# Performance work log

Hardware: AMD Instinct MI355X
Metric: run time of the kernel (lower is better)

## Reference

```python
import jax, jax.numpy as jnp
import numpy as np

DOF = 7
HID = 30
L_DIM = DOF * (DOF + 1) // 2  # 28
BATCH = 262144


def _linear_params(key, d_in, d_out, scale=0.3):
    k1, k2 = jax.random.split(key)
    W = jax.random.normal(k1, (d_out, d_in), dtype=jnp.float32) * scale / np.sqrt(d_in)
    b = jax.random.normal(k2, (d_out,), dtype=jnp.float32) * 0.01
    return W, b


def setup_inputs() -> dict:
    key = jax.random.key(0)
    ks = jax.random.split(key, 11)
    x = jax.random.normal(ks[0], (BATCH, 3 * DOF), dtype=jnp.float32)
    ld_w1, ld_b1 = _linear_params(ks[1], DOF, HID)
    ld_w2, ld_b2 = _linear_params(ks[2], HID, DOF)
    lo_w1, lo_b1 = _linear_params(ks[3], DOF, HID)
    lo_w2, lo_b2 = _linear_params(ks[4], HID, L_DIM - DOF)
    g_w1, g_b1 = _linear_params(ks[5], DOF, HID)
    g_w2, g_b2 = _linear_params(ks[6], HID, DOF)
    m_w1, m_b1 = _linear_params(ks[7], L_DIM + DOF, HID)
    m_w2, m_b2 = _linear_params(ks[8], HID, DOF)
    c_w1, c_b1 = _linear_params(ks[9], L_DIM * DOF + DOF, HID)
    c_w2, c_b2 = _linear_params(ks[10], HID, DOF)
    return dict(x=x,
                ld_w1=ld_w1, ld_b1=ld_b1, ld_w2=ld_w2, ld_b2=ld_b2,
                lo_w1=lo_w1, lo_b1=lo_b1, lo_w2=lo_w2, lo_b2=lo_b2,
                g_w1=g_w1, g_b1=g_b1, g_w2=g_w2, g_b2=g_b2,
                m_w1=m_w1, m_b1=m_b1, m_w2=m_w2, m_b2=m_b2,
                c_w1=c_w1, c_b1=c_b1, c_w2=c_w2, c_b2=c_b2)


def _sin_net_with_jac(q, W1, b1, W2, b2):
    # 2-layer SinNet: out = W2 @ sin(W1 q + b1) + b2, plus analytic batched Jacobian.
    pre = q @ W1.T + b1                 # [B, H]
    out = jnp.sin(pre) @ W2.T + b2      # [B, O]
    # d out_o / d q_d = sum_h W2[o,h] * cos(pre)[b,h] * W1[h,d]
    jac = jnp.einsum('oh,bh,hd->bod', W2, jnp.cos(pre), W1)  # [B, O, DOF]
    return out, jac


def _sigmoid_net(z, W1, b1, W2, b2):
    return jax.nn.sigmoid(z @ W1.T + b1) @ W2.T + b2


def reference(x,
              ld_w1, ld_b1, ld_w2, ld_b2,
              lo_w1, lo_b1, lo_w2, lo_b2,
              g_w1, g_b1, g_w2, g_b2,
              m_w1, m_b1, m_w2, m_b2,
              c_w1, c_b1, c_w2, c_b2):
    q = x[:, :DOF]
    qDot = x[:, DOF:2 * DOF]
    qDDot = x[:, 2 * DOF:3 * DOF]

    h_ld, jac_ld = _sin_net_with_jac(q, ld_w1, ld_b1, ld_w2, ld_b2)  # [B,DOF], [B,DOF,DOF]
    h_lo, jac_lo = _sin_net_with_jac(q, lo_w1, lo_b1, lo_w2, lo_b2)  # [B,L-D], [B,L-D,DOF]

    h_l = jnp.concatenate([h_ld, h_lo], axis=1)          # [B, L_DIM]
    m = _sigmoid_net(jnp.concatenate([h_l, qDDot], axis=1), m_w1, m_b1, m_w2, m_b2)

    # dl[:, i*DOF:(i+1)*DOF] = d h_l[:, i] / d q  -> flatten [B, L_DIM, DOF]
    dl = jnp.concatenate([jac_ld, jac_lo], axis=1).reshape(x.shape[0], L_DIM * DOF)
    c = _sigmoid_net(jnp.concatenate([dl, qDot], axis=1), c_w1, c_b1, c_w2, c_b2)

    g = jnp.sin(q @ g_w1.T + g_b1) @ g_w2.T + g_b2
    return m + c + g
```

## Files before the change

kernel.cpp:

```cpp
#include <hip/hip_runtime.h>


#define NT 256

typedef short bf16x8 __attribute__((ext_vector_type(8)));
typedef float f32x4  __attribute__((ext_vector_type(4)));

__device__ inline unsigned short f2b(float f) {
    union { float f; unsigned u; } v; v.f = f;
    return (unsigned short)((v.u + 0x7FFF + ((v.u >> 16) & 1)) >> 16);
}
__device__ inline unsigned pk2(float lo, float hi) {
    return (unsigned)f2b(lo) | ((unsigned)f2b(hi) << 16);
}

#define INV2PI 0.15915494309189535f

constexpr int PW_LD = 0;
constexpr int PW_LO = 1024;
constexpr int PW_G  = 2048;
constexpr int PB_MZ = 3072;
constexpr int PB_CZ = 6144;
constexpr int PB_O  = 9216;
constexpr int NPACK = 10752;

__global__ void precompute_kernel(
    const float* __restrict__ ld_w1, const float* __restrict__ ld_b1,
    const float* __restrict__ ld_w2, const float* __restrict__ ld_b2,
    const float* __restrict__ lo_w1, const float* __restrict__ lo_b1,
    const float* __restrict__ lo_w2, const float* __restrict__ lo_b2,
    const float* __restrict__ g_w1,  const float* __restrict__ g_b1,
    const float* __restrict__ g_w2,  const float* __restrict__ g_b2,
    const float* __restrict__ m_w1,  const float* __restrict__ m_b1,
    const float* __restrict__ m_w2,  const float* __restrict__ m_b2,
    const float* __restrict__ c_w1,  const float* __restrict__ c_b1,
    const float* __restrict__ c_w2,  const float* __restrict__ c_b2,
    float* __restrict__ ws)
{
    int i = blockIdx.x * blockDim.x + threadIdx.x;
    if (i < 16) { ws[i] = (i < 7) ? (m_b2[i] + c_b2[i] + g_b2[i]) : 0.f; return; }
    int r = i - 16;
    if (r >= NPACK) return;
    unsigned short* wp = (unsigned short*)ws + 32;
    float val = 0.f;
    if (r < 3072) {
        int tb = r / 1024, rr = r % 1024;
        int nc = rr >> 9, n = (rr >> 5) & 15, k = rr & 31, h = nc * 16 + n;
        const float* W1 = (tb == 0) ? ld_w1 : (tb == 1) ? lo_w1 : g_w1;
        const float* B1 = (tb == 0) ? ld_b1 : (tb == 1) ? lo_b1 : g_b1;
        if (h < 30) { if (k < 7) val = W1[h*7 + k]; else if (k == 7) val = B1[h]; }
    } else if (r < 6144) {
        int rr = r - 3072; int kc = rr >> 10; rr &= 1023;
        int nc = rr >> 9, n = (rr >> 5) & 15, k = rr & 31, j = nc * 16 + n;
        if (j < 30) {
            if (kc == 0) {
                if (k < 30) { float a = 0.f;
                    for (int o = 0; o < 7; ++o) a += m_w1[j*35 + o] * ld_w2[o*30 + k];
                    val = a; }
            } else if (kc == 1) {
                if (k < 30) { float a = 0.f;
                    for (int o = 0; o < 21; ++o) a += m_w1[j*35 + 7 + o] * lo_w2[o*30 + k];
                    val = a; }
            } else {
                if (k < 7) val = m_w1[j*35 + 28 + k];
                else if (k == 7) { float a = m_b1[j];
                    for (int o = 0; o < 7;  ++o) a += m_w1[j*35 + o]     * ld_b2[o];
                    for (int o = 0; o < 21; ++o) a += m_w1[j*35 + 7 + o] * lo_b2[o];
                    val = a; }
            }
        }
    } else if (r < 9216) {
        int rr = r - 6144; int kc = rr >> 10; rr &= 1023;
        int nc = rr >> 9, n = (rr >> 5) & 15, k = rr & 31, j = nc * 16 + n;
        if (j < 30) {
            if (kc == 0) {
                if (k < 30) { float a = 0.f;
                    for (int o = 0; o < 7; ++o) { float t = 0.f;
                        for (int d = 0; d < 7; ++d) t += c_w1[j*203 + o*7 + d] * ld_w1[k*7 + d];
                        a += ld_w2[o*30 + k] * t; }
                    val = a; }
            } else if (kc == 1) {
                if (k < 30) { float a = 0.f;
                    for (int o = 0; o < 21; ++o) { float t = 0.f;
                        for (int d = 0; d < 7; ++d) t += c_w1[j*203 + (7+o)*7 + d] * lo_w1[k*7 + d];
                        a += lo_w2[o*30 + k] * t; }
                    val = a; }
            } else {
                if (k < 7) val = c_w1[j*203 + 196 + k];
                else if (k == 7) val = c_b1[j];
            }
        }
    } else {
        int rr = r - 9216; int kc = rr >> 9, n = (rr >> 5) & 15, k = rr & 31;
        if (n < 7 && k < 30)
            val = ((kc == 0) ? m_w2 : (kc == 1) ? c_w2 : g_w2)[n*30 + k];
    }
    wp[r] = f2b(val);
}

#define MFMA(a, b, c) __builtin_amdgcn_mfma_f32_16x16x32_bf16((a), (b), (c), 0, 0, 0)

__global__ __launch_bounds__(NT, 3) void delan_main(
    const float* __restrict__ x, const float* __restrict__ ws, float* __restrict__ out)
{
    __shared__ __align__(16) unsigned short xs2[NT * 24 + 32];
    __shared__ __align__(16) unsigned short Lbuf[4 * 3968];

    const int tid = threadIdx.x;
    const int lane = tid & 63, wid = tid >> 6;
    const int n15 = lane & 15, quad = lane >> 4;

    {
        const float* xp = x + (size_t)(blockIdx.x * NT + tid) * 21;
        float v[21];
#pragma unroll
        for (int d = 0; d < 21; ++d) v[d] = xp[d];
        int4* dst = (int4*)(xs2 + tid * 24);
#pragma unroll
        for (int g = 0; g < 3; ++g) {
            int4 u;
            u.x = (int)pk2(v[g*7 + 0], v[g*7 + 1]);
            u.y = (int)pk2(v[g*7 + 2], v[g*7 + 3]);
            u.z = (int)pk2(v[g*7 + 4], v[g*7 + 5]);
            u.w = (int)pk2(v[g*7 + 6], 1.0f);
            dst[g] = u;
        }
    }
    if (tid < 16) ((unsigned*)(xs2 + NT * 24))[tid] = 0;
    __syncthreads();

    unsigned short* Ls = Lbuf + wid * 3968;
    unsigned short* Lc = Ls + 1152;
    unsigned short* Lg = Ls + 2304;

    const unsigned short* wp = (const unsigned short*)ws + 32;
    const int fo = n15 * 32 + quad * 8;

    bf16x8 bw_ld[2], bw_lo[2], bw_g[2], bm[3][2], bc[3][2], bo[3];
#pragma unroll
    for (int c = 0; c < 2; ++c) {
        bw_ld[c] = *(const bf16x8*)(wp + PW_LD + c*512 + fo);
        bw_lo[c] = *(const bf16x8*)(wp + PW_LO + c*512 + fo);
        bw_g[c]  = *(const bf16x8*)(wp + PW_G  + c*512 + fo);
#pragma unroll
        for (int kc = 0; kc < 3; ++kc) {
            bm[kc][c] = *(const bf16x8*)(wp + PB_MZ + kc*1024 + c*512 + fo);
            bc[kc][c] = *(const bf16x8*)(wp + PB_CZ + kc*1024 + c*512 + fo);
        }
    }
#pragma unroll
    for (int kc = 0; kc < 3; ++kc)
        bo[kc] = *(const bf16x8*)(wp + PB_O + kc*512 + fo);
    const float bout = ws[n15];

    const f32x4 zero4 = {0.f, 0.f, 0.f, 0.f};

    f32x4 pld[2], plo[2], pg[2];

    {
        const unsigned short* ep0 = xs2 + (wid * 64 + n15) * 24;
        bf16x8 a0 = *(const bf16x8*)(ep0 + quad * 8);
#pragma unroll
        for (int c = 0; c < 2; ++c) {
            pld[c] = MFMA(a0, bw_ld[c], zero4);
            plo[c] = MFMA(a0, bw_lo[c], zero4);
            pg[c]  = MFMA(a0, bw_g[c],  zero4);
        }
    }

#pragma unroll
    for (int t = 0; t < 4; ++t) {
        const int elb = wid * 64 + t * 16;
        const unsigned short* ep = xs2 + (elb + n15) * 24;

#pragma unroll
        for (int c = 0; c < 2; ++c) {
            const int h = c * 16 + n15;
#pragma unroll
            for (int rg = 0; rg < 4; ++rg) {
                const int m = quad * 4 + rg;
                float r1 = pld[c][rg] * INV2PI;
                Ls[m*72 + h]       = f2b(__builtin_amdgcn_sinf(r1));
                Lc[m*72 + h]       = f2b(__builtin_amdgcn_cosf(r1));
                float r2 = plo[c][rg] * INV2PI;
                Ls[m*72 + 32 + h]  = f2b(__builtin_amdgcn_sinf(r2));
                Lc[m*72 + 32 + h]  = f2b(__builtin_amdgcn_cosf(r2));
                Lg[m*104 + 64 + h] = f2b(__builtin_amdgcn_sinf(pg[c][rg] * INV2PI));
            }
        }

        if (t < 3) {
            const unsigned short* epn = xs2 + (elb + 16 + n15) * 24;
            bf16x8 a0n = *(const bf16x8*)(epn + quad * 8);
#pragma unroll
            for (int c = 0; c < 2; ++c) {
                pld[c] = MFMA(a0n, bw_ld[c], zero4);
                plo[c] = MFMA(a0n, bw_lo[c], zero4);
                pg[c]  = MFMA(a0n, bw_g[c],  zero4);
            }
        }

        bf16x8 as0 = *(const bf16x8*)(Ls + n15*72 + quad*8);
        bf16x8 as1 = *(const bf16x8*)(Ls + n15*72 + 32 + quad*8);
        bf16x8 ac0 = *(const bf16x8*)(Lc + n15*72 + quad*8);
        bf16x8 ac1 = *(const bf16x8*)(Lc + n15*72 + 32 + quad*8);
        bf16x8 aqd = *(const bf16x8*)(ep + 8 + quad * 8);
        bf16x8 add = *(const bf16x8*)(ep + 16 + quad * 8);

        f32x4 mz[2], cz[2];
#pragma unroll
        for (int c = 0; c < 2; ++c) {
            f32x4 m_ = MFMA(as0, bm[0][c], zero4);
            m_ = MFMA(as1, bm[1][c], m_);
            mz[c] = MFMA(add, bm[2][c], m_);
            f32x4 c_ = MFMA(ac0, bc[0][c], zero4);
            c_ = MFMA(ac1, bc[1][c], c_);
            cz[c] = MFMA(aqd, bc[2][c], c_);
        }

#pragma unroll
        for (int c = 0; c < 2; ++c) {
            const int j = c * 16 + n15;
#pragma unroll
            for (int rg = 0; rg < 4; ++rg) {
                const int m = quad * 4 + rg;
                Lg[m*104 + j]      = f2b(__builtin_amdgcn_rcpf(1.f + __expf(-mz[c][rg])));
                Lg[m*104 + 32 + j] = f2b(__builtin_amdgcn_rcpf(1.f + __expf(-cz[c][rg])));
            }
        }

        bf16x8 ag0 = *(const bf16x8*)(Lg + n15*104 + quad*8);
        bf16x8 ag1 = *(const bf16x8*)(Lg + n15*104 + 32 + quad*8);
        bf16x8 ag2 = *(const bf16x8*)(Lg + n15*104 + 64 + quad*8);
        f32x4 o = MFMA(ag0, bo[0], zero4);
        o = MFMA(ag1, bo[1], o);
        o = MFMA(ag2, bo[2], o);

        if (n15 < 7) {
            const int eb = blockIdx.x * NT + elb;
            float* op = out + (size_t)(eb + quad * 4) * 7 + n15;
            op[0]  = o[0] + bout;
            op[7]  = o[1] + bout;
            op[14] = o[2] + bout;
            op[21] = o[3] + bout;
        }
    }
}

extern "C" void kernel_launch(void* const* d_in, const int* in_sizes, int n_in,
                              void* d_out, int out_size, void* d_ws, size_t ws_size,
                              hipStream_t stream)
{
    const float* x = (const float*)d_in[0];
    float* ws = (float*)d_ws;

    precompute_kernel<<<(16 + NPACK + 255) / 256, 256, 0, stream>>>(
        (const float*)d_in[1],  (const float*)d_in[2],
        (const float*)d_in[3],  (const float*)d_in[4],
        (const float*)d_in[5],  (const float*)d_in[6],
        (const float*)d_in[7],  (const float*)d_in[8],
        (const float*)d_in[9],  (const float*)d_in[10],
        (const float*)d_in[11], (const float*)d_in[12],
        (const float*)d_in[13], (const float*)d_in[14],
        (const float*)d_in[15], (const float*)d_in[16],
        (const float*)d_in[17], (const float*)d_in[18],
        (const float*)d_in[19], (const float*)d_in[20],
        ws);

    const int batch = out_size / 7;
    const int nblk  = batch / NT;
    delan_main<<<nblk, NT, 0, stream>>>(x, ws, (float*)d_out);
}
```

Before: 132.1 us.

## Use single-wave blocks and drop software-pipelined first-layer MFMAs

Shrinks each block from four waves to one wave of 64 threads, so each block stages only its own 64 rows and owns one LDS scratch region. The loop over 16-row tiles is no longer unrolled, and the first-layer MFMAs for the next tile are no longer issued ahead of the current tile's sin/cos work. The aim is lower register and LDS pressure and higher occupancy, at the cost of losing the MFMA/transcendental overlap and adding loop overhead. Launch bounds change to four blocks per CU minimum.

```diff
diff --git a/kernel.cpp b/kernel.cpp
--- a/kernel.cpp
+++ b/kernel.cpp
@@ -1,7 +1,7 @@
 #include <hip/hip_runtime.h>
 
 
-#define NT 256
+#define NT 64
 
 typedef short bf16x8 __attribute__((ext_vector_type(8)));
 typedef float f32x4  __attribute__((ext_vector_type(4)));
@@ -100,22 +100,21 @@
 
 #define MFMA(a, b, c) __builtin_amdgcn_mfma_f32_16x16x32_bf16((a), (b), (c), 0, 0, 0)
 
-__global__ __launch_bounds__(NT, 3) void delan_main(
+__global__ __launch_bounds__(NT, 4) void delan_main(
     const float* __restrict__ x, const float* __restrict__ ws, float* __restrict__ out)
 {
     __shared__ __align__(16) unsigned short xs2[NT * 24 + 32];
-    __shared__ __align__(16) unsigned short Lbuf[4 * 3968];
-
-    const int tid = threadIdx.x;
-    const int lane = tid & 63, wid = tid >> 6;
+    __shared__ __align__(16) unsigned short Lbuf[3968];
+
+    const int lane = threadIdx.x;
     const int n15 = lane & 15, quad = lane >> 4;
 
     {
-        const float* xp = x + (size_t)(blockIdx.x * NT + tid) * 21;
+        const float* xp = x + (size_t)(blockIdx.x * NT + lane) * 21;
         float v[21];
 #pragma unroll
         for (int d = 0; d < 21; ++d) v[d] = xp[d];
-        int4* dst = (int4*)(xs2 + tid * 24);
+        int4* dst = (int4*)(xs2 + lane * 24);
 #pragma unroll
         for (int g = 0; g < 3; ++g) {
             int4 u;
@@ -126,10 +125,10 @@
             dst[g] = u;
         }
     }
-    if (tid < 16) ((unsigned*)(xs2 + NT * 24))[tid] = 0;
+    if (lane < 16) ((unsigned*)(xs2 + NT * 24))[lane] = 0;
     __syncthreads();
 
-    unsigned short* Ls = Lbuf + wid * 3968;
+    unsigned short* Ls = Lbuf;
     unsigned short* Lc = Ls + 1152;
     unsigned short* Lg = Ls + 2304;
 
@@ -155,23 +154,19 @@
 
     const f32x4 zero4 = {0.f, 0.f, 0.f, 0.f};
 
-    f32x4 pld[2], plo[2], pg[2];
-
-    {
-        const unsigned short* ep0 = xs2 + (wid * 64 + n15) * 24;
-        bf16x8 a0 = *(const bf16x8*)(ep0 + quad * 8);
+#pragma unroll 1
+    for (int t = 0; t < 4; ++t) {
+        const int elb = t * 16;
+        const unsigned short* ep = xs2 + (elb + n15) * 24;
+
+        bf16x8 a0 = *(const bf16x8*)(ep + quad * 8);
+        f32x4 pld[2], plo[2], pg[2];
 #pragma unroll
         for (int c = 0; c < 2; ++c) {
             pld[c] = MFMA(a0, bw_ld[c], zero4);
             plo[c] = MFMA(a0, bw_lo[c], zero4);
             pg[c]  = MFMA(a0, bw_g[c],  zero4);
         }
-    }
-
-#pragma unroll
-    for (int t = 0; t < 4; ++t) {
-        const int elb = wid * 64 + t * 16;
-        const unsigned short* ep = xs2 + (elb + n15) * 24;
 
 #pragma unroll
         for (int c = 0; c < 2; ++c) {
@@ -186,17 +181,6 @@
                 Ls[m*72 + 32 + h]  = f2b(__builtin_amdgcn_sinf(r2));
                 Lc[m*72 + 32 + h]  = f2b(__builtin_amdgcn_cosf(r2));
                 Lg[m*104 + 64 + h] = f2b(__builtin_amdgcn_sinf(pg[c][rg] * INV2PI));
-            }
-        }
-
-        if (t < 3) {
-            const unsigned short* epn = xs2 + (elb + 16 + n15) * 24;
-            bf16x8 a0n = *(const bf16x8*)(epn + quad * 8);
-#pragma unroll
-            for (int c = 0; c < 2; ++c) {
-                pld[c] = MFMA(a0n, bw_ld[c], zero4);
-                plo[c] = MFMA(a0n, bw_lo[c], zero4);
-                pg[c]  = MFMA(a0n, bw_g[c],  zero4);
             }
         }
 
```

New measurement: 134.0 us. No clear change (+1.5%).
